# Kernel tuning notes

Measured on AMD Instinct MI355X. Metric: run time of the kernel, lower is better.

## Reference

```python
import jax, jax.numpy as jnp
import numpy as np

BN_EPS = 1e-5
VQ_TEMP = 0.1

B, K, D_AUDIO, D_TEXT, VOCAB = 256, 8, 768, 512, 49408


def setup_inputs() -> dict:
    key = jax.random.key(0)
    k1, k2, k3, k4, k5 = jax.random.split(key, 5)
    return {
        "audio_kw": jax.random.normal(k1, (B, K, D_AUDIO), dtype=jnp.float32),
        "W_proj": jax.random.normal(k2, (D_AUDIO, D_TEXT), dtype=jnp.float32) * 0.02,
        "b_proj": jnp.zeros((D_TEXT,), dtype=jnp.float32),
        "bn_gamma": jax.random.uniform(k3, (D_TEXT,), dtype=jnp.float32, minval=0.5, maxval=1.5),
        "bn_beta": jax.random.normal(k4, (D_TEXT,), dtype=jnp.float32) * 0.01,
        "emb": jax.random.normal(k5, (VOCAB, D_TEXT), dtype=jnp.float32) * 0.02,
    }


def reference(audio_kw, W_proj, b_proj, bn_gamma, bn_beta, emb):
    # keyword projection: [B,K,Da] @ [Da,Dt] -> [B,K,Dt]
    proj = jnp.einsum("bkd,de->bke", audio_kw, W_proj) + b_proj
    # Kw_BatchNorm: batchnorm over (batch, keyword) per text feature, affine
    mean = jnp.mean(proj, axis=(0, 1))
    var = jnp.var(proj, axis=(0, 1))
    bn = (proj - mean) * jax.lax.rsqrt(var + BN_EPS) * bn_gamma + bn_beta
    # cosine similarity against full vocab table (one fused normalize+GEMM,
    # equivalent to the per-keyword F.cosine_similarity loop in the original)
    bn_n = bn / jnp.linalg.norm(bn, axis=-1, keepdims=True)
    emb_n = emb / jnp.linalg.norm(emb, axis=-1, keepdims=True)
    cos_score = jnp.einsum("bke,ve->bkv", bn_n, emb_n)  # [B,K,V]
    # VQ: temperature softmax over the vocab, then soft lookup
    subword_prob = jax.nn.softmax(cos_score / VQ_TEMP, axis=-1)
    vq_keywords = jnp.einsum("bkv,ve->bke", subword_prob, emb)  # [B,K,Dt]
    return vq_keywords
```

## Files before the change

### kernel.cpp

```cpp
#include <hip/hip_runtime.h>
#include <stdint.h>

typedef unsigned short u16;
typedef _Float16 f16;
typedef __attribute__((ext_vector_type(8))) _Float16 f16x8;
typedef __attribute__((ext_vector_type(4))) float f32x4;

#define DA 768
#define DT 512
#define NV 49408
#define MTOT 2048
#define NB2 193
#define KS 16

__device__ __forceinline__ u16 f2h(float f) {
  return __builtin_bit_cast(u16, (f16)f);
}

__device__ __forceinline__ void gload16(const void* g, void* l) {
  __builtin_amdgcn_global_load_lds((const __attribute__((address_space(1))) void*)g,
                                   (__attribute__((address_space(3))) void*)l,
                                   16, 0, 0);
}
#define SBAR()   __builtin_amdgcn_s_barrier()
#define SCHED0() __builtin_amdgcn_sched_barrier(0)

__global__ __launch_bounds__(256) void k_proj(const float* __restrict__ A,
                                              const float* __restrict__ W,
                                              const float* __restrict__ bias,
                                              float* __restrict__ P) {
  __shared__ float As[16][72];
  __shared__ float Bs[16][72];
  const int m0 = blockIdx.x * 64, n0 = blockIdx.y * 64;
  const int t = threadIdx.x;
  const int ty = t >> 4, tx = t & 15;
  const int ar = t >> 2, ak = (t & 3) * 4;
  const int bk = t >> 4, bn = (t & 15) * 4;
  float acc[4][4] = {};
  for (int k0 = 0; k0 < DA; k0 += 16) {
    float4 av = *(const float4*)&A[(size_t)(m0 + ar) * DA + k0 + ak];
    float4 bv = *(const float4*)&W[(size_t)(k0 + bk) * DT + n0 + bn];
    __syncthreads();
    As[ak + 0][ar] = av.x; As[ak + 1][ar] = av.y;
    As[ak + 2][ar] = av.z; As[ak + 3][ar] = av.w;
    *(float4*)&Bs[bk][bn] = bv;
    __syncthreads();
#pragma unroll
    for (int kk = 0; kk < 16; ++kk) {
      float4 a4 = *(const float4*)&As[kk][ty * 4];
      float4 b4 = *(const float4*)&Bs[kk][tx * 4];
      float ae[4] = {a4.x, a4.y, a4.z, a4.w};
      float be[4] = {b4.x, b4.y, b4.z, b4.w};
#pragma unroll
      for (int i = 0; i < 4; ++i)
#pragma unroll
        for (int j = 0; j < 4; ++j) acc[i][j] = fmaf(ae[i], be[j], acc[i][j]);
    }
  }
#pragma unroll
  for (int i = 0; i < 4; ++i) {
    int row = m0 + ty * 4 + i;
    float4 o;
    o.x = acc[i][0] + bias[n0 + tx * 4 + 0];
    o.y = acc[i][1] + bias[n0 + tx * 4 + 1];
    o.z = acc[i][2] + bias[n0 + tx * 4 + 2];
    o.w = acc[i][3] + bias[n0 + tx * 4 + 3];
    *(float4*)&P[(size_t)row * DT + n0 + tx * 4] = o;
  }
}

__global__ __launch_bounds__(256) void k_stats(const float* __restrict__ P,
                                               float* __restrict__ pstat) {
  const int t = threadIdx.x;
  const int r0 = blockIdx.x * 32;
  float s0 = 0, q0 = 0, s1 = 0, q1 = 0;
  for (int r = r0; r < r0 + 32; ++r) {
    float x0 = P[(size_t)r * DT + t];
    float x1 = P[(size_t)r * DT + t + 256];
    s0 += x0; q0 += x0 * x0; s1 += x1; q1 += x1 * x1;
  }
  float* d = pstat + (size_t)blockIdx.x * 1024;
  d[t] = s0; d[t + 256] = s1; d[512 + t] = q0; d[768 + t] = q1;
}

__global__ __launch_bounds__(256) void k_stats2(const float* __restrict__ pstat,
                                                float* __restrict__ stats) {
  int c = blockIdx.x * 256 + threadIdx.x;
  float s = 0.f;
  for (int b = 0; b < 64; ++b) s += pstat[(size_t)b * 1024 + c];
  stats[c] = s;
}

__global__ __launch_bounds__(64) void k_bnnorm(const float* __restrict__ P,
                                               const float* __restrict__ stats,
                                               const float* __restrict__ gamma,
                                               const float* __restrict__ beta,
                                               u16* __restrict__ bnn) {
  const int r = blockIdx.x, l = threadIdx.x;
  float v[8];
  float ss = 0.f;
#pragma unroll
  for (int i = 0; i < 8; ++i) {
    int c = l * 8 + i;
    float mean = stats[c] * (1.f / MTOT);
    float var = stats[DT + c] * (1.f / MTOT) - mean * mean;
    float is = rsqrtf(var + 1e-5f);
    float x = (P[(size_t)r * DT + c] - mean) * is * gamma[c] + beta[c];
    v[i] = x; ss += x * x;
  }
#pragma unroll
  for (int off = 32; off > 0; off >>= 1) ss += __shfl_xor(ss, off);
  float rn = rsqrtf(ss);
  union { u16 u[8]; int4 q; } pk;
#pragma unroll
  for (int i = 0; i < 8; ++i) pk.u[i] = f2h(v[i] * rn);
  *(int4*)&bnn[(size_t)r * DT + l * 8] = pk.q;
}

__global__ __launch_bounds__(256) void k_embprep(const float* __restrict__ emb,
                                                 u16* __restrict__ embH,
                                                 float* __restrict__ invn) {
  const int w = threadIdx.x >> 6, l = threadIdx.x & 63;
  const int vrow = blockIdx.x * 4 + w;
  const float* src = emb + (size_t)vrow * DT + l * 8;
  float4 a = *(const float4*)src;
  float4 b = *(const float4*)(src + 4);
  float x[8] = {a.x, a.y, a.z, a.w, b.x, b.y, b.z, b.w};
  float ss = 0.f;
#pragma unroll
  for (int i = 0; i < 8; ++i) ss += x[i] * x[i];
#pragma unroll
  for (int off = 32; off > 0; off >>= 1) ss += __shfl_xor(ss, off);
  if (l == 0) invn[vrow] = rsqrtf(ss) * 10.0f;
  union { u16 u[8]; int4 q; } pk;
#pragma unroll
  for (int i = 0; i < 8; ++i) pk.u[i] = f2h(x[i]);
  *(int4*)&embH[(size_t)vrow * DT + l * 8] = pk.q;
}

__global__ __launch_bounds__(256) void k_embT(const float* __restrict__ emb,
                                              u16* __restrict__ embT) {
  __shared__ float tile[64][65];
  const int v0 = blockIdx.x * 64, d0 = blockIdx.y * 64;
  const int t = threadIdx.x;
  {
    const int r = t >> 4, c = (t & 15) * 4;
#pragma unroll
    for (int i = 0; i < 4; ++i) {
      float4 x = *(const float4*)&emb[(size_t)(v0 + r + i * 16) * DT + d0 + c];
      tile[r + i * 16][c + 0] = x.x; tile[r + i * 16][c + 1] = x.y;
      tile[r + i * 16][c + 2] = x.z; tile[r + i * 16][c + 3] = x.w;
    }
  }
  __syncthreads();
  {
    const int d = t >> 2;
    const int vc = (t & 3) * 16;
    union { u16 u[8]; int4 q; } p0, p1;
#pragma unroll
    for (int i = 0; i < 8; ++i) p0.u[i] = f2h(tile[vc + i][d]);
#pragma unroll
    for (int i = 0; i < 8; ++i) p1.u[i] = f2h(tile[vc + 8 + i][d]);
    u16* dst = embT + (size_t)(d0 + d) * NV + v0 + vc;
    *(int4*)dst = p0.q;
    *(int4*)(dst + 8) = p1.q;
  }
}


#define MFMA_BLK(IH, JH)                                                     \
  _Pragma("unroll")                                                          \
  for (int ii = 0; ii < 4; ++ii) {                                           \
    _Pragma("unroll")                                                        \
    for (int jj = 0; jj < 2; ++jj) {                                         \
      acc[(IH)*4+ii][(JH)*2+jj] = __builtin_amdgcn_mfma_f32_16x16x32_f16(    \
          af[ii][0], bf[jj][0], acc[(IH)*4+ii][(JH)*2+jj], 0, 0, 0);         \
      acc[(IH)*4+ii][(JH)*2+jj] = __builtin_amdgcn_mfma_f32_16x16x32_f16(    \
          af[ii][1], bf[jj][1], acc[(IH)*4+ii][(JH)*2+jj], 0, 0, 0);         \
    }                                                                        \
  }

__device__ __forceinline__ void gemm_kloop(const f16* __restrict__ A,
                                           const f16* __restrict__ B,
                                           int lda, int ldb, size_t kb,
                                           int NT, int m0, int n0,
                                           char* lds, int tid,
                                           f32x4 (&acc)[8][4]) {
  const int l = tid & 63, lr = l & 15, lg = l >> 4;
  const int w = tid >> 6, wm = w >> 2, wn = w & 3;
  const int r8 = tid >> 3;
  const int gs = (tid & 7) ^ (r8 & 7);
  const f16* aRow = A + (size_t)(m0 + r8) * lda + kb + gs * 8;
  const f16* bRow = B + (size_t)(n0 + r8) * ldb + kb + gs * 8;
  char* ldsA = lds;
  char* ldsB = lds + 65536;
  char* dstA = ldsA + tid * 16;
  char* dstB = ldsB + tid * 16;
  const int gx0 = ((lg ^ (lr & 7)) << 4);
  const int gx1 = (((4 + lg) ^ (lr & 7)) << 4);
  const int aoff = (wm * 128 + lr) * 128;
  const int boff = (wn * 64 + lr) * 128;

#define STA(sl, q, kt) gload16(aRow + (size_t)(q) * 64 * lda + (size_t)(kt) * 64, \
                               dstA + (sl) * 32768 + (q) * 8192)
#define STB(sl, h, ql, kt) gload16(bRow + (size_t)((h) * 128 + (ql) * 64) * ldb + (size_t)(kt) * 64, \
                                   dstB + (sl) * 32768 + (h) * 16384 + (ql) * 8192)
#define RDA(IH)                                                              \
  _Pragma("unroll")                                                          \
  for (int ii = 0; ii < 4; ++ii) {                                           \
    af[ii][0] = *(const f16x8*)(As + ((IH)*4+ii) * 2048 + aoff + gx0);       \
    af[ii][1] = *(const f16x8*)(As + ((IH)*4+ii) * 2048 + aoff + gx1);       \
  }
#define RDB(JH)                                                              \
  _Pragma("unroll")                                                          \
  for (int jj = 0; jj < 2; ++jj) {                                           \
    bf[jj][0] = *(const f16x8*)(Bs + ((JH)*2+jj) * 2048 + boff + gx0);       \
    bf[jj][1] = *(const f16x8*)(Bs + ((JH)*2+jj) * 2048 + boff + gx1);       \
  }

  STA(0, 0, 0); STA(0, 1, 0); STA(0, 2, 0); STA(0, 3, 0);
  STB(0, 0, 0, 0); STB(0, 0, 1, 0); STB(0, 1, 0, 0); STB(0, 1, 1, 0);
  if (NT > 1) {
    STA(1, 0, 1); STA(1, 2, 1); STA(1, 1, 1); STA(1, 3, 1);
    asm volatile("s_waitcnt vmcnt(4)" ::: "memory");
  } else {
    asm volatile("s_waitcnt vmcnt(0)" ::: "memory");
  }
  SCHED0();
  SBAR(); SCHED0();

  f16x8 af[4][2], bf[2][2];
  for (int t = 0; t < NT; ++t) {
    const int sl = t & 1, ns = sl ^ 1;
    char* As = ldsA + sl * 32768;
    char* Bs = ldsB + sl * 32768;
    const bool s1 = (t + 1 < NT), s2 = (t + 2 < NT);
    RDA(0); RDB(0);
    if (s1) { STB(ns, 0, 0, t + 1); STB(ns, 0, 1, t + 1); }
    SBAR();
    asm volatile("s_waitcnt lgkmcnt(0)" ::: "memory"); SCHED0();
    __builtin_amdgcn_s_setprio(1);
    MFMA_BLK(0, 0);
    __builtin_amdgcn_s_setprio(0);
    SBAR(); SCHED0();
    RDB(1);
    if (s1) { STB(ns, 1, 0, t + 1); STB(ns, 1, 1, t + 1); }
    SBAR();
    asm volatile("s_waitcnt lgkmcnt(0)" ::: "memory"); SCHED0();
    __builtin_amdgcn_s_setprio(1);
    MFMA_BLK(0, 1);
    __builtin_amdgcn_s_setprio(0);
    SBAR(); SCHED0();
    RDA(1);
    if (s2) { STA(sl, 0, t + 2); STA(sl, 2, t + 2); }
    SBAR();
    asm volatile("s_waitcnt lgkmcnt(0)" ::: "memory"); SCHED0();
    __builtin_amdgcn_s_setprio(1);
    MFMA_BLK(1, 1);
    __builtin_amdgcn_s_setprio(0);
    SBAR(); SCHED0();
    RDB(0);
    if (s2) { STA(sl, 1, t + 2); STA(sl, 3, t + 2); }
    SBAR();
    asm volatile("s_waitcnt lgkmcnt(0)" ::: "memory"); SCHED0();
    __builtin_amdgcn_s_setprio(1);
    MFMA_BLK(1, 0);
    __builtin_amdgcn_s_setprio(0);
    if (s2) asm volatile("s_waitcnt vmcnt(4)" ::: "memory");
    else    asm volatile("s_waitcnt vmcnt(0)" ::: "memory");
    SCHED0();
    SBAR(); SCHED0();
  }
#undef STA
#undef STB
#undef RDA
#undef RDB
}

__global__ __launch_bounds__(512, 2) void k_score(const f16* __restrict__ A,
                                                  const f16* __restrict__ Bt,
                                                  const float* __restrict__ invn,
                                                  u16* __restrict__ E,
                                                  float* __restrict__ lpart,
                                                  int row0, int CH) {
  extern __shared__ char lds[];
  const int t = threadIdx.x;
  const int l = t & 63, lr = l & 15, lg = l >> 4;
  const int w = t >> 6, wm = w >> 2, wn = w & 3;
  const int mB = CH >> 8;
  const int nwg = NB2 * mB;
  const int o = blockIdx.x + blockIdx.y * gridDim.x;
  const int qd = nwg >> 3, r = nwg & 7;
  const int xcd = o & 7, idx = o >> 3;
  const int v = (xcd < r ? xcd * (qd + 1) : r * (qd + 1) + (xcd - r) * qd) + idx;
  const int nb = v % NB2, by = v / NB2;
  const int n0 = nb * 256;
  const int mloc = by * 256;

  f32x4 acc[8][4];
#pragma unroll
  for (int i = 0; i < 8; ++i)
#pragma unroll
    for (int j = 0; j < 4; ++j) acc[i][j] = (f32x4){0.f, 0.f, 0.f, 0.f};

  gemm_kloop(A, Bt, DT, DT, 0, DT / 64, row0 + mloc, n0, lds, t, acc);

  float* psum = (float*)(lds + 131072);
  float inv_j[4];
#pragma unroll
  for (int j = 0; j < 4; ++j) inv_j[j] = invn[n0 + wn * 64 + j * 16 + lr];
#pragma unroll
  for (int i = 0; i < 8; ++i) {
#pragma unroll
    for (int rg = 0; rg < 4; ++rg) {
      int row = wm * 128 + i * 16 + lg * 4 + rg;
      float rs = 0.f;
#pragma unroll
      for (int j = 0; j < 4; ++j) {
        float e = __expf(acc[i][j][rg] * inv_j[j]);
        rs += e;
        int col = wn * 64 + j * 16 + lr;
        int g4 = col >> 3;
        *(u16*)(lds + row * 512 + ((g4 ^ lg) << 4) + (col & 7) * 2) = f2h(e);
      }
#pragma unroll
      for (int m = 1; m <= 8; m <<= 1) rs += __shfl_xor(rs, m);
      if (lr == 0) psum[w * 128 + i * 16 + lg * 4 + rg] = rs;
    }
  }
  __syncthreads();
#pragma unroll
  for (int cc = 0; cc < 16; ++cc) {
    int lin = cc * 512 + t;
    int row = lin >> 5, g4 = lin & 31;
    int4 vv = *(const int4*)(lds + row * 512 + ((g4 ^ ((row >> 2) & 3)) << 4));
    *(int4*)&E[(size_t)(mloc + row) * NV + n0 + g4 * 8] = vv;
  }
  if (t < 256) {
    int wmx = t >> 7, rl = t & 127;
    float s = psum[(wmx * 4 + 0) * 128 + rl] + psum[(wmx * 4 + 1) * 128 + rl] +
              psum[(wmx * 4 + 2) * 128 + rl] + psum[(wmx * 4 + 3) * 128 + rl];
    lpart[(size_t)nb * CH + mloc + t] = s;
  }
}

__global__ __launch_bounds__(512, 2) void k_pv(const f16* __restrict__ A,
                                               const f16* __restrict__ Bt,
                                               float* __restrict__ Op,
                                               int CH) {
  extern __shared__ char lds[];
  const int t = threadIdx.x;
  const int l = t & 63, lr = l & 15, lg = l >> 4;
  const int w = t >> 6, wm = w >> 2, wn = w & 3;
  const int n0 = blockIdx.x * 256;
  const int mloc = blockIdx.y * 256;
  const int z = blockIdx.z;
  const int g0 = z * 48 + (z < 4 ? z : 4);
  const int NT = 48 + (z < 4 ? 1 : 0);
  const size_t kb = (size_t)g0 * 64;

  f32x4 acc[8][4];
#pragma unroll
  for (int i = 0; i < 8; ++i)
#pragma unroll
    for (int j = 0; j < 4; ++j) acc[i][j] = (f32x4){0.f, 0.f, 0.f, 0.f};

  gemm_kloop(A, Bt, NV, NV, kb, NT, mloc, n0, lds, t, acc);

#pragma unroll
  for (int i = 0; i < 8; ++i)
#pragma unroll
    for (int j = 0; j < 4; ++j)
#pragma unroll
      for (int rg = 0; rg < 4; ++rg) {
        int row = mloc + wm * 128 + i * 16 + lg * 4 + rg;
        int col = n0 + wn * 64 + j * 16 + lr;
        Op[((size_t)z * CH + row) * DT + col] = acc[i][j][rg];
      }
}

__global__ __launch_bounds__(256) void k_lred(const float* __restrict__ lp,
                                              float* __restrict__ lv, int CH) {
  int rb = blockIdx.x * 256 + threadIdx.x;
  float s = 0.f;
  for (int nb = 0; nb < NB2; ++nb) s += lp[(size_t)nb * CH + rb];
  lv[rb] = s;
}

__global__ __launch_bounds__(256) void k_out(const float* __restrict__ Op,
                                             const float* __restrict__ lv,
                                             float* __restrict__ out,
                                             int row0, int CH) {
  int idx = blockIdx.x * 256 + threadIdx.x;
  int rb = idx >> 9, c = idx & 511;
  float s = 0.f;
#pragma unroll
  for (int zz = 0; zz < KS; ++zz) s += Op[((size_t)zz * CH + rb) * DT + c];
  out[(size_t)(row0 + rb) * DT + c] = s / lv[rb];
}

extern "C" void kernel_launch(void* const* d_in, const int* in_sizes, int n_in,
                              void* d_out, int out_size, void* d_ws, size_t ws_size,
                              hipStream_t stream) {
  const float* audio = (const float*)d_in[0];
  const float* W     = (const float*)d_in[1];
  const float* bias  = (const float*)d_in[2];
  const float* gamma = (const float*)d_in[3];
  const float* beta  = (const float*)d_in[4];
  const float* emb   = (const float*)d_in[5];
  float* out = (float*)d_out;

  char* ws = (char*)d_ws;
  size_t off = 0;
  auto alloc = [&](size_t bytes) {
    char* p = ws + off;
    off += (bytes + 255) & ~(size_t)255;
    return p;
  };
  float* proj  = (float*)alloc((size_t)MTOT * DT * 4);
  float* pstat = (float*)alloc((size_t)64 * 1024 * 4);
  float* stats = (float*)alloc((size_t)2 * DT * 4);
  u16*   bnnH  = (u16*)alloc((size_t)MTOT * DT * 2);
  u16*   embH  = (u16*)alloc((size_t)NV * DT * 2);
  u16*   embT  = (u16*)alloc((size_t)DT * NV * 2);
  float* invn  = (float*)alloc((size_t)NV * 4);
  size_t fixed_off = off;

  int CH = 2048;
  while (CH > 256) {
    size_t need = fixed_off;
    need += (((size_t)CH * NV * 2) + 255) & ~(size_t)255;
    need += (((size_t)NB2 * CH * 4) + 255) & ~(size_t)255;
    need += (((size_t)CH * 4) + 255) & ~(size_t)255;
    need += (((size_t)KS * CH * DT * 4) + 255) & ~(size_t)255;
    if (need <= ws_size) break;
    CH >>= 1;
  }
  u16*   E     = (u16*)alloc((size_t)CH * NV * 2);
  float* lpart = (float*)alloc((size_t)NB2 * CH * 4);
  float* lvec  = (float*)alloc((size_t)CH * 4);
  float* Op    = (float*)alloc((size_t)KS * CH * DT * 4);
  if (ws_size < off) return;

  hipFuncSetAttribute((const void*)k_score,
                      hipFuncAttributeMaxDynamicSharedMemorySize, 135168);
  hipFuncSetAttribute((const void*)k_pv,
                      hipFuncAttributeMaxDynamicSharedMemorySize, 131072);

  k_proj<<<dim3(32, 8), dim3(256), 0, stream>>>(audio, W, bias, proj);
  k_stats<<<dim3(64), dim3(256), 0, stream>>>(proj, pstat);
  k_stats2<<<dim3(4), dim3(256), 0, stream>>>(pstat, stats);
  k_bnnorm<<<dim3(MTOT), dim3(64), 0, stream>>>(proj, stats, gamma, beta, bnnH);
  k_embprep<<<dim3(NV / 4), dim3(256), 0, stream>>>(emb, embH, invn);
  k_embT<<<dim3(NV / 64, DT / 64), dim3(256), 0, stream>>>(emb, embT);

  for (int row0 = 0; row0 < MTOT; row0 += CH) {
    k_score<<<dim3(NB2, CH / 256), dim3(512), 135168, stream>>>(
        (const f16*)bnnH, (const f16*)embH, invn, E, lpart, row0, CH);
    k_lred<<<dim3(CH / 256), dim3(256), 0, stream>>>(lpart, lvec, CH);
    k_pv<<<dim3(2, CH / 256, KS), dim3(512), 131072, stream>>>(
        (const f16*)E, (const f16*)embT, Op, CH);
    k_out<<<dim3(CH * 2), dim3(256), 0, stream>>>(Op, lvec, out, row0, CH);
  }
}
```

Baseline: 435.3 us.

## Fuse embedding prep kernels and simplify GEMM k-loop pipeline

Merges the two embedding preprocessing kernels (fp16 copy plus inverse norm, and the transposed fp16 copy) into one kernel, so emb is read from global memory once instead of twice. It also replaces the hand-interleaved four-phase GEMM k-loop, which used setprio, split loads and two-ahead A prefetch, with a plain double-buffered loop that issues every next-tile load up front and waits on vmcnt(0) at the end of each iteration. The simpler loop may lose latency hiding and MFMA/LDS overlap in the dominant score and PV GEMMs. The fused prep kernel runs fewer blocks, each looping over the feature dimension.

```diff
diff --git a/kernel.cpp b/kernel.cpp
--- a/kernel.cpp
+++ b/kernel.cpp
@@ -24,6 +24,7 @@
 }
 #define SBAR()   __builtin_amdgcn_s_barrier()
 #define SCHED0() __builtin_amdgcn_sched_barrier(0)
+#define MFMA16(a, b, c) __builtin_amdgcn_mfma_f32_16x16x32_f16((a), (b), (c), 0, 0, 0)
 
 __global__ __launch_bounds__(256) void k_proj(const float* __restrict__ A,
                                               const float* __restrict__ W,
@@ -117,68 +118,47 @@
   *(int4*)&bnn[(size_t)r * DT + l * 8] = pk.q;
 }
 
-__global__ __launch_bounds__(256) void k_embprep(const float* __restrict__ emb,
-                                                 u16* __restrict__ embH,
-                                                 float* __restrict__ invn) {
-  const int w = threadIdx.x >> 6, l = threadIdx.x & 63;
-  const int vrow = blockIdx.x * 4 + w;
-  const float* src = emb + (size_t)vrow * DT + l * 8;
-  float4 a = *(const float4*)src;
-  float4 b = *(const float4*)(src + 4);
-  float x[8] = {a.x, a.y, a.z, a.w, b.x, b.y, b.z, b.w};
-  float ss = 0.f;
-#pragma unroll
-  for (int i = 0; i < 8; ++i) ss += x[i] * x[i];
-#pragma unroll
-  for (int off = 32; off > 0; off >>= 1) ss += __shfl_xor(ss, off);
-  if (l == 0) invn[vrow] = rsqrtf(ss) * 10.0f;
-  union { u16 u[8]; int4 q; } pk;
-#pragma unroll
-  for (int i = 0; i < 8; ++i) pk.u[i] = f2h(x[i]);
-  *(int4*)&embH[(size_t)vrow * DT + l * 8] = pk.q;
-}
-
-__global__ __launch_bounds__(256) void k_embT(const float* __restrict__ emb,
-                                              u16* __restrict__ embT) {
+__global__ __launch_bounds__(256) void k_embprep2(const float* __restrict__ emb,
+                                                  u16* __restrict__ embH,
+                                                  u16* __restrict__ embT,
+                                                  float* __restrict__ invn) {
   __shared__ float tile[64][65];
-  const int v0 = blockIdx.x * 64, d0 = blockIdx.y * 64;
+  const int v0 = blockIdx.x * 64;
   const int t = threadIdx.x;
-  {
-    const int r = t >> 4, c = (t & 15) * 4;
+  const int r = t >> 4, c4 = (t & 15) * 4;
+  const int vr = t >> 2, hc = (t & 3) * 16;
+  const int dr = t >> 2, vc = (t & 3) * 16;
+  float ssq = 0.f;
+  for (int d0 = 0; d0 < DT; d0 += 64) {
+    __syncthreads();
 #pragma unroll
     for (int i = 0; i < 4; ++i) {
-      float4 x = *(const float4*)&emb[(size_t)(v0 + r + i * 16) * DT + d0 + c];
-      tile[r + i * 16][c + 0] = x.x; tile[r + i * 16][c + 1] = x.y;
-      tile[r + i * 16][c + 2] = x.z; tile[r + i * 16][c + 3] = x.w;
-    }
-  }
-  __syncthreads();
-  {
-    const int d = t >> 2;
-    const int vc = (t & 3) * 16;
+      float4 x = *(const float4*)&emb[(size_t)(v0 + r + i * 16) * DT + d0 + c4];
+      tile[r + i * 16][c4 + 0] = x.x; tile[r + i * 16][c4 + 1] = x.y;
+      tile[r + i * 16][c4 + 2] = x.z; tile[r + i * 16][c4 + 3] = x.w;
+    }
+    __syncthreads();
+    union { u16 u[8]; int4 q; } pa, pb;
+#pragma unroll
+    for (int i = 0; i < 8; ++i) { float f = tile[vr][hc + i];     pa.u[i] = f2h(f); ssq += f * f; }
+#pragma unroll
+    for (int i = 0; i < 8; ++i) { float f = tile[vr][hc + 8 + i]; pb.u[i] = f2h(f); ssq += f * f; }
+    *(int4*)&embH[(size_t)(v0 + vr) * DT + d0 + hc] = pa.q;
+    *(int4*)&embH[(size_t)(v0 + vr) * DT + d0 + hc + 8] = pb.q;
     union { u16 u[8]; int4 q; } p0, p1;
 #pragma unroll
-    for (int i = 0; i < 8; ++i) p0.u[i] = f2h(tile[vc + i][d]);
-#pragma unroll
-    for (int i = 0; i < 8; ++i) p1.u[i] = f2h(tile[vc + 8 + i][d]);
-    u16* dst = embT + (size_t)(d0 + d) * NV + v0 + vc;
+    for (int i = 0; i < 8; ++i) p0.u[i] = f2h(tile[vc + i][dr]);
+#pragma unroll
+    for (int i = 0; i < 8; ++i) p1.u[i] = f2h(tile[vc + 8 + i][dr]);
+    u16* dst = embT + (size_t)(d0 + dr) * NV + v0 + vc;
     *(int4*)dst = p0.q;
     *(int4*)(dst + 8) = p1.q;
   }
-}
-
-
-#define MFMA_BLK(IH, JH)                                                     \
-  _Pragma("unroll")                                                          \
-  for (int ii = 0; ii < 4; ++ii) {                                           \
-    _Pragma("unroll")                                                        \
-    for (int jj = 0; jj < 2; ++jj) {                                         \
-      acc[(IH)*4+ii][(JH)*2+jj] = __builtin_amdgcn_mfma_f32_16x16x32_f16(    \
-          af[ii][0], bf[jj][0], acc[(IH)*4+ii][(JH)*2+jj], 0, 0, 0);         \
-      acc[(IH)*4+ii][(JH)*2+jj] = __builtin_amdgcn_mfma_f32_16x16x32_f16(    \
-          af[ii][1], bf[jj][1], acc[(IH)*4+ii][(JH)*2+jj], 0, 0, 0);         \
-    }                                                                        \
-  }
+  ssq += __shfl_xor(ssq, 1);
+  ssq += __shfl_xor(ssq, 2);
+  if ((t & 3) == 0) invn[v0 + vr] = rsqrtf(ssq) * 10.0f;
+}
+
 
 __device__ __forceinline__ void gemm_kloop(const f16* __restrict__ A,
                                            const f16* __restrict__ B,
@@ -203,78 +183,80 @@
 
 #define STA(sl, q, kt) gload16(aRow + (size_t)(q) * 64 * lda + (size_t)(kt) * 64, \
                                dstA + (sl) * 32768 + (q) * 8192)
-#define STB(sl, h, ql, kt) gload16(bRow + (size_t)((h) * 128 + (ql) * 64) * ldb + (size_t)(kt) * 64, \
-                                   dstB + (sl) * 32768 + (h) * 16384 + (ql) * 8192)
-#define RDA(IH)                                                              \
-  _Pragma("unroll")                                                          \
-  for (int ii = 0; ii < 4; ++ii) {                                           \
-    af[ii][0] = *(const f16x8*)(As + ((IH)*4+ii) * 2048 + aoff + gx0);       \
-    af[ii][1] = *(const f16x8*)(As + ((IH)*4+ii) * 2048 + aoff + gx1);       \
-  }
-#define RDB(JH)                                                              \
-  _Pragma("unroll")                                                          \
-  for (int jj = 0; jj < 2; ++jj) {                                           \
-    bf[jj][0] = *(const f16x8*)(Bs + ((JH)*2+jj) * 2048 + boff + gx0);       \
-    bf[jj][1] = *(const f16x8*)(Bs + ((JH)*2+jj) * 2048 + boff + gx1);       \
-  }
+#define STB(sl, q, kt) gload16(bRow + (size_t)(q) * 64 * ldb + (size_t)(kt) * 64, \
+                               dstB + (sl) * 32768 + (q) * 8192)
 
   STA(0, 0, 0); STA(0, 1, 0); STA(0, 2, 0); STA(0, 3, 0);
-  STB(0, 0, 0, 0); STB(0, 0, 1, 0); STB(0, 1, 0, 0); STB(0, 1, 1, 0);
-  if (NT > 1) {
-    STA(1, 0, 1); STA(1, 2, 1); STA(1, 1, 1); STA(1, 3, 1);
-    asm volatile("s_waitcnt vmcnt(4)" ::: "memory");
-  } else {
-    asm volatile("s_waitcnt vmcnt(0)" ::: "memory");
-  }
+  STB(0, 0, 0); STB(0, 1, 0); STB(0, 2, 0); STB(0, 3, 0);
+  asm volatile("s_waitcnt vmcnt(0)" ::: "memory");
   SCHED0();
   SBAR(); SCHED0();
 
-  f16x8 af[4][2], bf[2][2];
   for (int t = 0; t < NT; ++t) {
     const int sl = t & 1, ns = sl ^ 1;
-    char* As = ldsA + sl * 32768;
-    char* Bs = ldsB + sl * 32768;
-    const bool s1 = (t + 1 < NT), s2 = (t + 2 < NT);
-    RDA(0); RDB(0);
-    if (s1) { STB(ns, 0, 0, t + 1); STB(ns, 0, 1, t + 1); }
-    SBAR();
-    asm volatile("s_waitcnt lgkmcnt(0)" ::: "memory"); SCHED0();
-    __builtin_amdgcn_s_setprio(1);
-    MFMA_BLK(0, 0);
-    __builtin_amdgcn_s_setprio(0);
-    SBAR(); SCHED0();
-    RDB(1);
-    if (s1) { STB(ns, 1, 0, t + 1); STB(ns, 1, 1, t + 1); }
-    SBAR();
-    asm volatile("s_waitcnt lgkmcnt(0)" ::: "memory"); SCHED0();
-    __builtin_amdgcn_s_setprio(1);
-    MFMA_BLK(0, 1);
-    __builtin_amdgcn_s_setprio(0);
-    SBAR(); SCHED0();
-    RDA(1);
-    if (s2) { STA(sl, 0, t + 2); STA(sl, 2, t + 2); }
-    SBAR();
-    asm volatile("s_waitcnt lgkmcnt(0)" ::: "memory"); SCHED0();
-    __builtin_amdgcn_s_setprio(1);
-    MFMA_BLK(1, 1);
-    __builtin_amdgcn_s_setprio(0);
-    SBAR(); SCHED0();
-    RDB(0);
-    if (s2) { STA(sl, 1, t + 2); STA(sl, 3, t + 2); }
-    SBAR();
-    asm volatile("s_waitcnt lgkmcnt(0)" ::: "memory"); SCHED0();
-    __builtin_amdgcn_s_setprio(1);
-    MFMA_BLK(1, 0);
-    __builtin_amdgcn_s_setprio(0);
-    if (s2) asm volatile("s_waitcnt vmcnt(4)" ::: "memory");
-    else    asm volatile("s_waitcnt vmcnt(0)" ::: "memory");
+    const char* As = ldsA + sl * 32768;
+    const char* Bs = ldsB + sl * 32768;
+    if (t + 1 < NT) {
+      STA(ns, 0, t + 1); STA(ns, 1, t + 1); STA(ns, 2, t + 1); STA(ns, 3, t + 1);
+      STB(ns, 0, t + 1); STB(ns, 1, t + 1); STB(ns, 2, t + 1); STB(ns, 3, t + 1);
+    }
+    f16x8 a0[4][2], b0[2][2];
+#pragma unroll
+    for (int ii = 0; ii < 4; ++ii) {
+      a0[ii][0] = *(const f16x8*)(As + ii * 2048 + aoff + gx0);
+      a0[ii][1] = *(const f16x8*)(As + ii * 2048 + aoff + gx1);
+    }
+#pragma unroll
+    for (int jj = 0; jj < 2; ++jj) {
+      b0[jj][0] = *(const f16x8*)(Bs + jj * 2048 + boff + gx0);
+      b0[jj][1] = *(const f16x8*)(Bs + jj * 2048 + boff + gx1);
+    }
+#pragma unroll
+    for (int ii = 0; ii < 4; ++ii)
+#pragma unroll
+      for (int jj = 0; jj < 2; ++jj) {
+        acc[ii][jj] = MFMA16(a0[ii][0], b0[jj][0], acc[ii][jj]);
+        acc[ii][jj] = MFMA16(a0[ii][1], b0[jj][1], acc[ii][jj]);
+      }
+    f16x8 b1[2][2];
+#pragma unroll
+    for (int jj = 0; jj < 2; ++jj) {
+      b1[jj][0] = *(const f16x8*)(Bs + (2 + jj) * 2048 + boff + gx0);
+      b1[jj][1] = *(const f16x8*)(Bs + (2 + jj) * 2048 + boff + gx1);
+    }
+#pragma unroll
+    for (int ii = 0; ii < 4; ++ii)
+#pragma unroll
+      for (int jj = 0; jj < 2; ++jj) {
+        acc[ii][2 + jj] = MFMA16(a0[ii][0], b1[jj][0], acc[ii][2 + jj]);
+        acc[ii][2 + jj] = MFMA16(a0[ii][1], b1[jj][1], acc[ii][2 + jj]);
+      }
+    f16x8 a1[4][2];
+#pragma unroll
+    for (int ii = 0; ii < 4; ++ii) {
+      a1[ii][0] = *(const f16x8*)(As + (4 + ii) * 2048 + aoff + gx0);
+      a1[ii][1] = *(const f16x8*)(As + (4 + ii) * 2048 + aoff + gx1);
+    }
+#pragma unroll
+    for (int ii = 0; ii < 4; ++ii)
+#pragma unroll
+      for (int jj = 0; jj < 2; ++jj) {
+        acc[4 + ii][2 + jj] = MFMA16(a1[ii][0], b1[jj][0], acc[4 + ii][2 + jj]);
+        acc[4 + ii][2 + jj] = MFMA16(a1[ii][1], b1[jj][1], acc[4 + ii][2 + jj]);
+      }
+#pragma unroll
+    for (int ii = 0; ii < 4; ++ii)
+#pragma unroll
+      for (int jj = 0; jj < 2; ++jj) {
+        acc[4 + ii][jj] = MFMA16(a1[ii][0], b0[jj][0], acc[4 + ii][jj]);
+        acc[4 + ii][jj] = MFMA16(a1[ii][1], b0[jj][1], acc[4 + ii][jj]);
+      }
+    asm volatile("s_waitcnt vmcnt(0)" ::: "memory");
     SCHED0();
     SBAR(); SCHED0();
   }
 #undef STA
 #undef STB
-#undef RDA
-#undef RDB
 }
 
 __global__ __launch_bounds__(512, 2) void k_score(const f16* __restrict__ A,
@@ -451,8 +433,7 @@
   k_stats<<<dim3(64), dim3(256), 0, stream>>>(proj, pstat);
   k_stats2<<<dim3(4), dim3(256), 0, stream>>>(pstat, stats);
   k_bnnorm<<<dim3(MTOT), dim3(64), 0, stream>>>(proj, stats, gamma, beta, bnnH);
-  k_embprep<<<dim3(NV / 4), dim3(256), 0, stream>>>(emb, embH, invn);
-  k_embT<<<dim3(NV / 64, DT / 64), dim3(256), 0, stream>>>(emb, embT);
+  k_embprep2<<<dim3(NV / 64), dim3(256), 0, stream>>>(emb, embH, embT, invn);
 
   for (int row0 = 0; row0 < MTOT; row0 += CH) {
     k_score<<<dim3(NB2, CH / 256), dim3(512), 135168, stream>>>(
```

After: 435.0 us. Within noise of the previous version (-0.1%).
